# Kernel optimization log

Measured on AMD Instinct MI355X. Metric: run time of the kernel, lower is better.

The kernel has to match this reference:

```python
import jax, jax.numpy as jnp
import numpy as np

C_IN = 256   # in_channels
D = 256      # hidden_dim
RNN_OUT = 2 * D  # bidir concat
K = 80       # num_classes - 1
B, H, W = 16, 64, 64


def setup_inputs() -> dict:
    key = jax.random.key(0)
    ks = jax.random.split(key, 32)
    sD = 1.0 / np.sqrt(D)
    sR = 1.0 / np.sqrt(RNN_OUT)
    f32 = jnp.float32
    inp = {}
    inp["feat"] = jax.random.normal(ks[0], (B, C_IN, H, W), f32)
    # 1x1 conv projection (acts as per-pixel linear)
    inp["proj_w"] = jax.random.normal(ks[1], (D, C_IN), f32) * sD
    inp["proj_b"] = jnp.zeros((D,), f32)
    # FastRNN forward-direction cell
    inp["Wf"] = jax.random.normal(ks[2], (D, D), f32) * sD
    inp["Uf"] = jax.random.normal(ks[3], (D, D), f32) * sD
    inp["bf"] = jnp.zeros((D,), f32)
    inp["alpha_f"] = jnp.asarray(-3.0, f32)  # sigmoid(-3) ~ 0.05 (FastRNN init)
    inp["beta_f"] = jnp.asarray(3.0, f32)    # sigmoid(3)  ~ 0.95
    # FastRNN backward-direction cell
    inp["Wb"] = jax.random.normal(ks[4], (D, D), f32) * sD
    inp["Ub"] = jax.random.normal(ks[5], (D, D), f32) * sD
    inp["bb"] = jnp.zeros((D,), f32)
    inp["alpha_b"] = jnp.asarray(-3.0, f32)
    inp["beta_b"] = jnp.asarray(3.0, f32)
    # cls MLP: Linear(RNN_OUT,RNN_OUT) -> ReLU -> Linear(RNN_OUT,K)
    inp["cls_w1"] = jax.random.normal(ks[6], (RNN_OUT, RNN_OUT), f32) * sR
    inp["cls_b1"] = jnp.zeros((RNN_OUT,), f32)
    inp["cls_w2"] = jax.random.normal(ks[7], (K, RNN_OUT), f32) * sR
    inp["cls_b2"] = jnp.zeros((K,), f32)
    # reg MLP -> 4
    inp["reg_w1"] = jax.random.normal(ks[8], (RNN_OUT, RNN_OUT), f32) * sR
    inp["reg_b1"] = jnp.zeros((RNN_OUT,), f32)
    inp["reg_w2"] = jax.random.normal(ks[9], (4, RNN_OUT), f32) * sR
    inp["reg_b2"] = jnp.zeros((4,), f32)
    # ctr MLP -> 1
    inp["ctr_w1"] = jax.random.normal(ks[10], (RNN_OUT, RNN_OUT), f32) * sR
    inp["ctr_b1"] = jnp.zeros((RNN_OUT,), f32)
    inp["ctr_w2"] = jax.random.normal(ks[11], (1, RNN_OUT), f32) * sR
    inp["ctr_b2"] = jnp.zeros((1,), f32)
    return inp


def _fastrnn_scan(pre, U, alpha, beta):
    # pre: (S, B, D) = W x_t + b precomputed for all steps
    a = jax.nn.sigmoid(alpha)
    b = jax.nn.sigmoid(beta)
    def step(h, p):
        h_new = a * jnp.tanh(p + h @ U.T) + b * h
        return h_new, h_new
    h0 = jnp.zeros(pre.shape[1:], pre.dtype)
    _, hs = jax.lax.scan(step, h0, pre)
    return hs  # (S, B, D)


def _mlp(h, w1, b1, w2, b2):
    return jax.nn.relu(h @ w1.T + b1) @ w2.T + b2


def reference(feat, proj_w, proj_b, Wf, Uf, bf, alpha_f, beta_f,
              Wb, Ub, bb, alpha_b, beta_b,
              cls_w1, cls_b1, cls_w2, cls_b2,
              reg_w1, reg_b1, reg_w2, reg_b2,
              ctr_w1, ctr_b1, ctr_w2, ctr_b2):
    Bn, C, Hn, Wn = feat.shape
    # 1x1 conv proj then flatten spatial tokens: (B, S, D)
    x = jnp.einsum('bchw,dc->bhwd', feat, proj_w) + proj_b
    x = x.reshape(Bn, Hn * Wn, D)
    # forward-direction FastRNN
    pre_f = (x @ Wf.T + bf).transpose(1, 0, 2)           # (S, B, D)
    h_f = _fastrnn_scan(pre_f, Uf, alpha_f, beta_f).transpose(1, 0, 2)
    # backward-direction FastRNN
    pre_b = (x[:, ::-1] @ Wb.T + bb).transpose(1, 0, 2)
    h_b = _fastrnn_scan(pre_b, Ub, alpha_b, beta_b).transpose(1, 0, 2)[:, ::-1]
    h = jnp.concatenate([h_f, h_b], axis=-1)             # (B, S, 2D)
    cls = _mlp(h, cls_w1, cls_b1, cls_w2, cls_b2)
    reg = _mlp(h, reg_w1, reg_b1, reg_w2, reg_b2)
    ctr = _mlp(h, ctr_w1, ctr_b1, ctr_w2, ctr_b2)
    cls = cls.reshape(Bn, Hn, Wn, K).transpose(0, 3, 1, 2)
    reg = jax.nn.relu(reg.reshape(Bn, Hn, Wn, 4).transpose(0, 3, 1, 2))
    ctr = ctr.reshape(Bn, Hn, Wn, 1).transpose(0, 3, 1, 2)
    return (cls, reg, ctr)
```

## Files before the change

kernel.cpp:

```cpp
#include <hip/hip_runtime.h>
#include <hip/hip_bf16.h>

typedef short bf16x8 __attribute__((ext_vector_type(8)));
typedef float f32x4 __attribute__((ext_vector_type(4)));

__device__ __forceinline__ ushort f2b(float x) {
    __hip_bfloat16 h = __float2bfloat16(x);
    return *reinterpret_cast<ushort*>(&h);
}

__device__ __forceinline__ void gload_lds16(const void* g, void* l) {
    __builtin_amdgcn_global_load_lds(
        (const __attribute__((address_space(1))) void*)g,
        (__attribute__((address_space(3))) void*)l, 16, 0, 0);
}

__global__ __launch_bounds__(256) void prep_mcat(
    const float* __restrict__ proj_w, const float* __restrict__ proj_b,
    const float* __restrict__ Wf, const float* __restrict__ bf_,
    const float* __restrict__ Wb, const float* __restrict__ bb_,
    __hip_bfloat16* __restrict__ Mcat, float* __restrict__ cvec)
{
    int n = blockIdx.x;
    int c = threadIdx.x;
    const float* W    = (n < 256) ? (Wf + n * 256) : (Wb + (n - 256) * 256);
    const float* bias = (n < 256) ? bf_ : bb_;
    float acc = 0.f;
    for (int k = 0; k < 256; ++k)
        acc = fmaf(W[k], proj_w[k * 256 + c], acc);
    Mcat[n * 256 + c] = __float2bfloat16(acc);

    __shared__ float red[256];
    red[c] = W[c] * proj_b[c];
    __syncthreads();
    for (int s = 128; s > 0; s >>= 1) {
        if (c < s) red[c] += red[c + s];
        __syncthreads();
    }
    if (c == 0) cvec[n] = red[0] + bias[n & 255];
}

__global__ __launch_bounds__(256) void prep_weights(
    const float* __restrict__ cls_w1, const float* __restrict__ cls_b1,
    const float* __restrict__ cls_w2, const float* __restrict__ cls_b2,
    const float* __restrict__ reg_w1, const float* __restrict__ reg_b1,
    const float* __restrict__ reg_w2, const float* __restrict__ reg_b2,
    const float* __restrict__ ctr_w1, const float* __restrict__ ctr_b1,
    const float* __restrict__ ctr_w2, const float* __restrict__ ctr_b2,
    __hip_bfloat16* __restrict__ W1cat, float* __restrict__ b1cat,
    __hip_bfloat16* __restrict__ w2h, float* __restrict__ b2h)
{
    int idx = blockIdx.x * 256 + threadIdx.x;
    if (idx < 786432) {
        int n = idx >> 9, k = idx & 511;
        const float* src = (n < 512) ? cls_w1 : (n < 1024 ? reg_w1 : ctr_w1);
        int nn = n & 511;
        W1cat[idx] = __float2bfloat16(src[nn * 512 + k]);
    }
    if (idx < 65536) {
        int r = idx >> 9, k = idx & 511;
        float v = 0.f;
        if (r < 80)       v = cls_w2[r * 512 + k];
        else if (r < 84)  v = reg_w2[(r - 80) * 512 + k];
        else if (r == 96) v = ctr_w2[k];
        w2h[idx] = __float2bfloat16(v);
    }
    if (idx < 1536)
        b1cat[idx] = (idx < 512) ? cls_b1[idx] : (idx < 1024 ? reg_b1[idx - 512] : ctr_b1[idx - 1024]);
    if (idx < 112)
        b2h[idx] = (idx < 80) ? cls_b2[idx] : (idx < 84 ? reg_b2[idx - 80] : (idx == 96 ? ctr_b2[0] : 0.f));
}

__global__ __launch_bounds__(256) void transpose_feat(
    const float* __restrict__ feat, __hip_bfloat16* __restrict__ fx)
{
    __shared__ float tile[32][65];
    int st = blockIdx.x * 64, ct = blockIdx.y * 32, b = blockIdx.z;
    int tid = threadIdx.x;
    int sl = tid & 63, cl = tid >> 6;
    const float* fp = feat + ((size_t)b * 256 + ct) * 4096 + st;
#pragma unroll
    for (int i = 0; i < 8; ++i)
        tile[cl + i * 4][sl] = fp[(size_t)(cl + i * 4) * 4096 + sl];
    __syncthreads();
    int cw = tid & 31, sw = tid >> 5;
#pragma unroll
    for (int i = 0; i < 8; ++i) {
        int ss = st + sw + i * 8;
        fx[((size_t)ss * 16 + b) * 256 + ct + cw] = __float2bfloat16(tile[cw][sw + i * 8]);
    }
}

template <int MODE>
__global__ __launch_bounds__(256) void gemm_bf16(
    const __hip_bfloat16* __restrict__ A, const __hip_bfloat16* __restrict__ B,
    void* __restrict__ Cv, const float* __restrict__ bias, int M, int N, int K)
{
    __shared__ __align__(16) ushort As[128][64];
    __shared__ __align__(16) ushort Bs[128][64];
    const int tid = threadIdx.x;
    const int wv = tid >> 6;
    const int lane = tid & 63;
    const int wm = wv >> 1, wn = wv & 1;
    const int l15 = lane & 15, l4 = lane >> 4;
    const int m0 = blockIdx.y * 128;
    const int n0 = blockIdx.x * 128;

    f32x4 acc[4][4];
#pragma unroll
    for (int i = 0; i < 4; ++i)
#pragma unroll
        for (int j = 0; j < 4; ++j) acc[i][j] = (f32x4){0.f, 0.f, 0.f, 0.f};

    const int c0 = wv * 4 * 64 + lane;
    const ushort* Abase = (const ushort*)A;
    const ushort* Bbase = (const ushort*)B;

    for (int k0 = 0; k0 < K; k0 += 64) {
#pragma unroll
        for (int i = 0; i < 4; ++i) {
            int c = c0 + i * 64;
            int row = c >> 3, kc = c & 7;
            int kcs = (kc ^ (row & 7)) * 8;
            gload_lds16(Abase + (size_t)(m0 + row) * K + k0 + kcs,
                        &As[0][0] + (wv * 4 + i) * 512);
            gload_lds16(Bbase + (size_t)(n0 + row) * K + k0 + kcs,
                        &Bs[0][0] + (wv * 4 + i) * 512);
        }
        asm volatile("s_waitcnt vmcnt(0)" ::: "memory");
        __syncthreads();

#pragma unroll
        for (int ks = 0; ks < 2; ++ks) {
            const int swz = ((ks * 4 + l4) ^ (l15 & 7)) * 8;
            bf16x8 af[4], bf[4];
#pragma unroll
            for (int mi = 0; mi < 4; ++mi)
                af[mi] = *(const bf16x8*)(&As[0][0] + (wm * 64 + mi * 16 + l15) * 64 + swz);
#pragma unroll
            for (int ni = 0; ni < 4; ++ni)
                bf[ni] = *(const bf16x8*)(&Bs[0][0] + (wn * 64 + ni * 16 + l15) * 64 + swz);
#pragma unroll
            for (int mi = 0; mi < 4; ++mi)
#pragma unroll
                for (int ni = 0; ni < 4; ++ni)
                    acc[mi][ni] = __builtin_amdgcn_mfma_f32_16x16x32_bf16(af[mi], bf[ni], acc[mi][ni], 0, 0, 0);
        }
        __syncthreads();
    }

#pragma unroll
    for (int mi = 0; mi < 4; ++mi) {
#pragma unroll
        for (int ni = 0; ni < 4; ++ni) {
            int col = n0 + wn * 64 + ni * 16 + l15;
#pragma unroll
            for (int r = 0; r < 4; ++r) {
                int row = m0 + wm * 64 + mi * 16 + l4 * 4 + r;
                float v = acc[mi][ni][r];
                if constexpr (MODE >= 1) v += bias[col];
                if constexpr (MODE == 2) {
                    v = fmaxf(v, 0.f);
                    ((__hip_bfloat16*)Cv)[(size_t)row * N + col] = __float2bfloat16(v);
                } else {
                    ((float*)Cv)[(size_t)row * N + col] = v;
                }
            }
        }
    }
}

__global__ __launch_bounds__(512) void fused_l2(
    const __hip_bfloat16* __restrict__ L1c, const __hip_bfloat16* __restrict__ w2h,
    const float* __restrict__ b2h, float* __restrict__ out, int chunk)
{
    __shared__ __align__(16) char smem[256 * 105 * 4];
    ushort* As = (ushort*)smem;
    ushort* Bs = (ushort*)(smem + 32768);
    float* sacc = (float*)smem;

    const int tid = threadIdx.x;
    const int wv = tid >> 6;
    const int lane = tid & 63;
    const int l15 = lane & 15, l4 = lane >> 4;
    const int tok0 = blockIdx.x * 256;
    const ushort* Ab = (const ushort*)L1c;
    const ushort* Bb = (const ushort*)w2h;

    f32x4 acc[2][7];
#pragma unroll
    for (int i = 0; i < 2; ++i)
#pragma unroll
        for (int j = 0; j < 7; ++j) acc[i][j] = (f32x4){0.f, 0.f, 0.f, 0.f};

#pragma unroll
    for (int p = 0; p < 3; ++p) {
        for (int k0 = 0; k0 < 512; k0 += 64) {
#pragma unroll
            for (int i = 0; i < 4; ++i) {
                int c = (wv * 4 + i) * 64 + lane;
                int row = c >> 3, kc = c & 7;
                int kcs = (kc ^ (row & 7)) * 8;
                gload_lds16(Ab + (size_t)(tok0 + row) * 1536 + p * 512 + k0 + kcs, As + c * 8);
            }
#pragma unroll
            for (int i = 0; i < 2; ++i) {
                int c = (wv * 2 + i) * 64 + lane;
                int row = c >> 3, kc = c & 7;
                int kcs = (kc ^ (row & 7)) * 8;
                gload_lds16(Bb + (size_t)row * 512 + k0 + kcs, Bs + c * 8);
            }
            asm volatile("s_waitcnt vmcnt(0)" ::: "memory");
            __syncthreads();

#pragma unroll
            for (int ks = 0; ks < 2; ++ks) {
                const int swz = ((ks * 4 + l4) ^ (l15 & 7)) * 8;
                bf16x8 af0 = *(const bf16x8*)(As + (wv * 32 + l15) * 64 + swz);
                bf16x8 af1 = *(const bf16x8*)(As + (wv * 32 + 16 + l15) * 64 + swz);
                if (p == 0) {
#pragma unroll
                    for (int ni = 0; ni < 5; ++ni) {
                        bf16x8 bf = *(const bf16x8*)(Bs + (ni * 16 + l15) * 64 + swz);
                        acc[0][ni] = __builtin_amdgcn_mfma_f32_16x16x32_bf16(af0, bf, acc[0][ni], 0, 0, 0);
                        acc[1][ni] = __builtin_amdgcn_mfma_f32_16x16x32_bf16(af1, bf, acc[1][ni], 0, 0, 0);
                    }
                } else {
                    const int ni = (p == 1) ? 5 : 6;
                    bf16x8 bf = *(const bf16x8*)(Bs + (ni * 16 + l15) * 64 + swz);
                    acc[0][ni] = __builtin_amdgcn_mfma_f32_16x16x32_bf16(af0, bf, acc[0][ni], 0, 0, 0);
                    acc[1][ni] = __builtin_amdgcn_mfma_f32_16x16x32_bf16(af1, bf, acc[1][ni], 0, 0, 0);
                }
            }
            __syncthreads();
        }
    }

#pragma unroll
    for (int mi = 0; mi < 2; ++mi) {
#pragma unroll
        for (int ni = 0; ni < 7; ++ni) {
            const int fragcol = ni * 16 + l15;
            const float bias = b2h[fragcol];
#pragma unroll
            for (int r = 0; r < 4; ++r) {
                int row = wv * 32 + mi * 16 + l4 * 4 + r;
                float v = acc[mi][ni][r] + bias;
                if (ni == 5 && l15 < 4) v = fmaxf(v, 0.f);
                if (ni < 6) sacc[row * 105 + fragcol] = v;
                else if (l15 == 0) sacc[row * 105 + 96] = v;
            }
        }
    }
    __syncthreads();

    const int s0 = chunk * 2048 + blockIdx.x * 16;
#pragma unroll
    for (int it = 0; it < 10; ++it) {
        int slot = it * 512 + tid;
        int j = slot >> 6;
        int rem = slot & 63;
        int b = rem >> 2, q = rem & 3;
        float4 v;
#pragma unroll
        for (int e = 0; e < 4; ++e)
            ((float*)&v)[e] = sacc[((q * 4 + e) * 16 + b) * 105 + j];
        *(float4*)(out + (size_t)b * 327680 + (size_t)j * 4096 + s0 + q * 4) = v;
    }
    if (tid < 256) {
        int j = tid >> 6, rem = tid & 63, b = rem >> 2, q = rem & 3;
        float4 v;
#pragma unroll
        for (int e = 0; e < 4; ++e)
            ((float*)&v)[e] = sacc[((q * 4 + e) * 16 + b) * 105 + 80 + j];
        *(float4*)(out + 5242880 + (size_t)b * 16384 + (size_t)j * 4096 + s0 + q * 4) = v;
    }
    if (tid < 64) {
        int b = tid >> 2, q = tid & 3;
        float4 v;
#pragma unroll
        for (int e = 0; e < 4; ++e)
            ((float*)&v)[e] = sacc[((q * 4 + e) * 16 + b) * 105 + 96];
        *(float4*)(out + 5505024 + (size_t)b * 4096 + s0 + q * 4) = v;
    }
}

#define HROW 264
#define CHUNK_S 32
#define WARMUP 192
__global__ __launch_bounds__(512, 2) void scan_chunk(
    const float* __restrict__ pre, const float* __restrict__ Uf, const float* __restrict__ Ub,
    const float* __restrict__ alpha_f, const float* __restrict__ beta_f,
    const float* __restrict__ alpha_b, const float* __restrict__ beta_b,
    __hip_bfloat16* __restrict__ h_out)
{
    const int dir = blockIdx.y;
    const int chk = blockIdx.x;
    const int o0 = chk * CHUNK_S;
    const int o1 = o0 + CHUNK_S;
    int start = o0 - WARMUP; if (start < 0) start = 0;

    const int tid = threadIdx.x;
    const int w = tid >> 6;
    const int lane = tid & 63;
    const int l15 = lane & 15;
    const int l4 = lane >> 4;

    const float* U = dir ? Ub : Uf;
    const float alpha = dir ? alpha_b[0] : alpha_f[0];
    const float beta  = dir ? beta_b[0]  : beta_f[0];
    const float a  = 1.f / (1.f + __expf(-alpha));
    const float bd = 1.f / (1.f + __expf(-beta));

    bf16x8 ufr[2][8];
#pragma unroll
    for (int mt = 0; mt < 2; ++mt) {
        const int row = w * 32 + mt * 16 + l15;
#pragma unroll
        for (int kc = 0; kc < 8; ++kc) {
            const float* up = U + (size_t)row * 256 + kc * 32 + l4 * 8;
            bf16x8 fr;
#pragma unroll
            for (int j = 0; j < 8; ++j) fr[j] = (short)f2b(up[j]);
            ufr[mt][kc] = fr;
        }
    }

    __shared__ __align__(16) ushort hbuf[2][16][HROW];
    for (int i = tid; i < 2 * 16 * HROW; i += 512) ((ushort*)hbuf)[i] = 0;

    float4 hown[2];
    hown[0] = (float4){0.f, 0.f, 0.f, 0.f};
    hown[1] = (float4){0.f, 0.f, 0.f, 0.f};

    const size_t off0 = (size_t)l15 * 512 + dir * 256 + w * 32 + l4 * 4;

    const int wb = tid >> 5;
    const int wp = tid & 31;
    ushort* hob = (ushort*)h_out + dir * 256 + (size_t)wb * 512 + wp * 8;

    const int sA0 = dir ? (4095 - start) : start;
    const int sB0 = dir ? (4095 - (start + 1)) : (start + 1);
    float4 pA0 = *(const float4*)(pre + (size_t)sA0 * 8192 + off0);
    float4 pA1 = *(const float4*)(pre + (size_t)sA0 * 8192 + off0 + 16);
    float4 pB0 = *(const float4*)(pre + (size_t)sB0 * 8192 + off0);
    float4 pB1 = *(const float4*)(pre + (size_t)sB0 * 8192 + off0 + 16);

    __syncthreads();

#define SCAN_STEP(T, CUR, NXT, P0, P1)                                              \
    do {                                                                            \
        const int s_ = dir ? (4095 - (T)) : (T);                                    \
        bf16x8 bfrag[8];                                                            \
        _Pragma("unroll")                                                           \
        for (int kc = 0; kc < 8; ++kc)                                              \
            bfrag[kc] = *(const bf16x8*)&hbuf[CUR][l15][kc * 32 + l4 * 8];          \
        f32x4 acc0 = (f32x4){0.f, 0.f, 0.f, 0.f};                                   \
        f32x4 acc1 = (f32x4){0.f, 0.f, 0.f, 0.f};                                   \
        _Pragma("unroll")                                                           \
        for (int kc = 0; kc < 8; ++kc) {                                            \
            acc0 = __builtin_amdgcn_mfma_f32_16x16x32_bf16(ufr[0][kc], bfrag[kc], acc0, 0, 0, 0); \
            acc1 = __builtin_amdgcn_mfma_f32_16x16x32_bf16(ufr[1][kc], bfrag[kc], acc1, 0, 0, 0); \
        }                                                                           \
        _Pragma("unroll")                                                           \
        for (int mt = 0; mt < 2; ++mt) {                                            \
            f32x4 accv = mt ? acc1 : acc0;                                          \
            const float* pcp = mt ? (const float*)&(P1) : (const float*)&(P0);      \
            const float* hop_ = (const float*)&hown[mt];                            \
            float hn[4];                                                            \
            _Pragma("unroll")                                                       \
            for (int r = 0; r < 4; ++r) {                                           \
                float z = accv[r] + pcp[r];                                         \
                float e = exp2f(z * 2.885390081777927f);                            \
                float th = fmaf(-2.f, __builtin_amdgcn_rcpf(e + 1.f), 1.f);         \
                hn[r] = fmaf(a, th, bd * hop_[r]);                                  \
            }                                                                       \
            hown[mt] = (float4){hn[0], hn[1], hn[2], hn[3]};                        \
            ushort4 pk;                                                             \
            pk.x = f2b(hn[0]); pk.y = f2b(hn[1]); pk.z = f2b(hn[2]); pk.w = f2b(hn[3]); \
            *(ushort4*)&hbuf[NXT][l15][w * 32 + mt * 16 + l4 * 4] = pk;             \
        }                                                                           \
        asm volatile("s_waitcnt lgkmcnt(0)" ::: "memory");                          \
        __builtin_amdgcn_s_barrier();                                               \
        if ((T) >= o0) {                                                            \
            bf16x8 hv = *(const bf16x8*)&hbuf[NXT][wb][wp * 8];                     \
            *(bf16x8*)(hob + (size_t)s_ * 8192) = hv;                               \
        }                                                                           \
    } while (0)

    for (int t = start; t < o1; t += 2) {
        SCAN_STEP(t, 0, 1, pA0, pA1);
        {
            int t2 = (t + 2 < o1) ? (t + 2) : (o1 - 1);
            int s2 = dir ? (4095 - t2) : t2;
            pA0 = *(const float4*)(pre + (size_t)s2 * 8192 + off0);
            pA1 = *(const float4*)(pre + (size_t)s2 * 8192 + off0 + 16);
        }
        SCAN_STEP(t + 1, 1, 0, pB0, pB1);
        {
            int t3 = (t + 3 < o1) ? (t + 3) : (o1 - 1);
            int s3 = dir ? (4095 - t3) : t3;
            pB0 = *(const float4*)(pre + (size_t)s3 * 8192 + off0);
            pB1 = *(const float4*)(pre + (size_t)s3 * 8192 + off0 + 16);
        }
    }
#undef SCAN_STEP
}

extern "C" void kernel_launch(void* const* d_in, const int* in_sizes, int n_in,
                              void* d_out, int out_size, void* d_ws, size_t ws_size,
                              hipStream_t stream) {
    (void)in_sizes; (void)n_in; (void)out_size; (void)ws_size;
    const float* feat    = (const float*)d_in[0];
    const float* proj_w  = (const float*)d_in[1];
    const float* proj_b  = (const float*)d_in[2];
    const float* Wf      = (const float*)d_in[3];
    const float* Uf      = (const float*)d_in[4];
    const float* bf_     = (const float*)d_in[5];
    const float* alpha_f = (const float*)d_in[6];
    const float* beta_f  = (const float*)d_in[7];
    const float* Wb      = (const float*)d_in[8];
    const float* Ub      = (const float*)d_in[9];
    const float* bb_     = (const float*)d_in[10];
    const float* alpha_b = (const float*)d_in[11];
    const float* beta_b  = (const float*)d_in[12];
    const float* cls_w1  = (const float*)d_in[13];
    const float* cls_b1  = (const float*)d_in[14];
    const float* cls_w2  = (const float*)d_in[15];
    const float* cls_b2  = (const float*)d_in[16];
    const float* reg_w1  = (const float*)d_in[17];
    const float* reg_b1  = (const float*)d_in[18];
    const float* reg_w2  = (const float*)d_in[19];
    const float* reg_b2  = (const float*)d_in[20];
    const float* ctr_w1  = (const float*)d_in[21];
    const float* ctr_b1  = (const float*)d_in[22];
    const float* ctr_w2  = (const float*)d_in[23];
    const float* ctr_b2  = (const float*)d_in[24];

    char* ws = (char*)d_ws;
    __hip_bfloat16* h_bf  = (__hip_bfloat16*)(ws);
    float*          pre   = (float*)(ws + 67108864);
    __hip_bfloat16* L1c   = (__hip_bfloat16*)(ws + 67108864);
    char*           regC  = ws + 201326592;
    __hip_bfloat16* fx    = (__hip_bfloat16*)regC;
    char*           wts   = ws + 260046848;
    __hip_bfloat16* Mcat  = (__hip_bfloat16*)(wts);
    float*          cvec  = (float*)(wts + 262144);
    __hip_bfloat16* W1cat = (__hip_bfloat16*)(wts + 264192);
    float*          b1cat = (float*)(wts + 1837056);
    __hip_bfloat16* w2h   = (__hip_bfloat16*)(wts + 1843200);
    float*          b2h   = (float*)(wts + 1974272);

    prep_mcat<<<512, 256, 0, stream>>>(proj_w, proj_b, Wf, bf_, Wb, bb_, Mcat, cvec);
    prep_weights<<<3072, 256, 0, stream>>>(cls_w1, cls_b1, cls_w2, cls_b2,
        reg_w1, reg_b1, reg_w2, reg_b2, ctr_w1, ctr_b1, ctr_w2, ctr_b2,
        W1cat, b1cat, w2h, b2h);
    transpose_feat<<<dim3(64, 8, 16), 256, 0, stream>>>(feat, fx);

    gemm_bf16<1><<<dim3(4, 512), 256, 0, stream>>>(fx, Mcat, pre, cvec, 65536, 512, 256);

    scan_chunk<<<dim3(128, 2), 512, 0, stream>>>(pre, Uf, Ub, alpha_f, beta_f, alpha_b, beta_b, h_bf);

    for (int c = 0; c < 2; ++c) {
        gemm_bf16<2><<<dim3(12, 256), 256, 0, stream>>>(
            h_bf + (size_t)c * 32768 * 512, W1cat, L1c, b1cat, 32768, 1536, 512);
        fused_l2<<<128, 512, 0, stream>>>(L1c, w2h, b2h, (float*)d_out, c);
    }
}
```

Before: 467.1 us.

## Add 256x256-tile pipelined bf16 GEMM with fused ReLU for MLP layer 1

Replaces the generic 128x128-tile GEMM for the first MLP layer with a dedicated 512-thread kernel that uses 256x256 output tiles, XOR-swizzled LDS staging through direct global-to-LDS loads, half-tile double buffering interleaved with MFMA phases, and a workgroup index swizzle for L2 locality. The goal is more data reuse per LDS load and better overlap of global loads with MFMA compute on the dominant GEMM (32768x1536x512, run twice). In exchange it holds many more accumulator registers and relies on hand-placed waitcnt and barrier scheduling, which is fragile.

```diff
diff --git a/kernel.cpp b/kernel.cpp
--- a/kernel.cpp
+++ b/kernel.cpp
@@ -165,6 +165,136 @@
                 } else {
                     ((float*)Cv)[(size_t)row * N + col] = v;
                 }
+            }
+        }
+    }
+}
+
+__global__ __launch_bounds__(512, 2) void gemm256_relu(
+    const __hip_bfloat16* __restrict__ A, const __hip_bfloat16* __restrict__ B,
+    __hip_bfloat16* __restrict__ C, const float* __restrict__ bias, int N, int K)
+{
+    __shared__ __align__(16) ushort Asm[2][2][128][64];
+    __shared__ __align__(16) ushort Bsm[2][2][128][64];
+    const int tid = threadIdx.x;
+    const int wv = tid >> 6;
+    const int lane = tid & 63;
+    const int wqm = wv >> 2, wqn = wv & 3;
+    const int l15 = lane & 15, l4 = lane >> 4;
+    const int nt = K >> 6;
+
+    const int nbx = gridDim.x;
+    int wg = blockIdx.y * nbx + blockIdx.x;
+    int cpx = (nbx * gridDim.y) >> 3;
+    int swz = (wg & 7) * cpx + (wg >> 3);
+    const int m0 = (swz / nbx) * 256;
+    const int n0 = (swz % nbx) * 256;
+
+    f32x4 acc[8][4];
+#pragma unroll
+    for (int i = 0; i < 8; ++i)
+#pragma unroll
+        for (int j = 0; j < 4; ++j) acc[i][j] = (f32x4){0.f, 0.f, 0.f, 0.f};
+
+    const ushort* Ab = (const ushort*)A;
+    const ushort* Bb = (const ushort*)B;
+
+#define STG_HALF(MEM, P, G0, TILE, HALF)                                            \
+    do { if ((TILE) < nt) {                                                         \
+        ushort* db_ = &MEM[(TILE) & 1][HALF][0][0];                                 \
+        _Pragma("unroll")                                                           \
+        for (int i_ = 0; i_ < 2; ++i_) {                                            \
+            int c_ = (wv * 2 + i_) * 64 + lane;                                     \
+            int r_ = c_ >> 3, kc_ = c_ & 7;                                         \
+            int kcs_ = (kc_ ^ (r_ & 7)) * 8;                                        \
+            gload_lds16(P + (size_t)((G0) + (HALF) * 128 + r_) * K + (TILE) * 64 + kcs_, \
+                        db_ + c_ * 8);                                              \
+        } } } while (0)
+
+#define PH(DBUF, MH, NH, ENDW, ...)                                                 \
+    do {                                                                            \
+        bf16x8 afr[2][4], bfr[2][2];                                                \
+        _Pragma("unroll")                                                           \
+        for (int ks_ = 0; ks_ < 2; ++ks_) {                                         \
+            _Pragma("unroll")                                                       \
+            for (int fm_ = 0; fm_ < 4; ++fm_) {                                     \
+                int r_ = wqm * 64 + fm_ * 16 + l15;                                 \
+                afr[ks_][fm_] = *(const bf16x8*)&Asm[DBUF][MH][r_][((ks_ * 4 + l4) ^ (r_ & 7)) * 8]; \
+            }                                                                       \
+            _Pragma("unroll")                                                       \
+            for (int fn_ = 0; fn_ < 2; ++fn_) {                                     \
+                int r_ = wqn * 32 + fn_ * 16 + l15;                                 \
+                bfr[ks_][fn_] = *(const bf16x8*)&Bsm[DBUF][NH][r_][((ks_ * 4 + l4) ^ (r_ & 7)) * 8]; \
+            }                                                                       \
+        }                                                                           \
+        __VA_ARGS__;                                                                \
+        asm volatile("" ::: "memory");                                              \
+        __builtin_amdgcn_s_barrier();                                               \
+        asm volatile("s_waitcnt lgkmcnt(0)" ::: "memory");                          \
+        __builtin_amdgcn_sched_barrier(0);                                          \
+        __builtin_amdgcn_s_setprio(1);                                              \
+        _Pragma("unroll")                                                           \
+        for (int ks_ = 0; ks_ < 2; ++ks_)                                           \
+            _Pragma("unroll")                                                       \
+            for (int fm_ = 0; fm_ < 4; ++fm_)                                       \
+                _Pragma("unroll")                                                   \
+                for (int fn_ = 0; fn_ < 2; ++fn_)                                   \
+                    acc[(MH) * 4 + fm_][(NH) * 2 + fn_] =                           \
+                        __builtin_amdgcn_mfma_f32_16x16x32_bf16(                    \
+                            afr[ks_][fm_], bfr[ks_][fn_],                           \
+                            acc[(MH) * 4 + fm_][(NH) * 2 + fn_], 0, 0, 0);          \
+        __builtin_amdgcn_s_setprio(0);                                              \
+        ENDW;                                                                       \
+        asm volatile("" ::: "memory");                                              \
+        __builtin_amdgcn_s_barrier();                                               \
+        asm volatile("" ::: "memory");                                              \
+    } while (0)
+
+#define VMW_STEADY asm volatile("s_waitcnt vmcnt(4)" ::: "memory")
+#define VMW_TAIL   asm volatile("s_waitcnt vmcnt(0)" ::: "memory")
+
+    STG_HALF(Asm, Ab, m0, 0, 0);
+    STG_HALF(Bsm, Bb, n0, 0, 0);
+    STG_HALF(Asm, Ab, m0, 0, 1);
+    STG_HALF(Bsm, Bb, n0, 0, 1);
+    STG_HALF(Asm, Ab, m0, 1, 0);
+    STG_HALF(Bsm, Bb, n0, 1, 0);
+    asm volatile("s_waitcnt vmcnt(4)" ::: "memory");
+    asm volatile("" ::: "memory");
+    __builtin_amdgcn_s_barrier();
+    asm volatile("" ::: "memory");
+
+    const int niter = nt >> 1;
+    for (int i = 0; i < niter; ++i) {
+        const int U = 2 * i, V = U + 1;
+        const bool tailA = (U + 2 >= nt), tailB = (V + 2 >= nt);
+        PH(0, 0, 0, , STG_HALF(Asm, Ab, m0, V, 1); STG_HALF(Bsm, Bb, n0, V, 1));
+        PH(0, 0, 1, , );
+        PH(0, 1, 0, , STG_HALF(Asm, Ab, m0, U + 2, 0));
+        if (tailA) { PH(0, 1, 1, VMW_TAIL, STG_HALF(Bsm, Bb, n0, U + 2, 0)); }
+        else       { PH(0, 1, 1, VMW_STEADY, STG_HALF(Bsm, Bb, n0, U + 2, 0)); }
+        PH(1, 0, 0, , STG_HALF(Asm, Ab, m0, U + 2, 1); STG_HALF(Bsm, Bb, n0, U + 2, 1));
+        PH(1, 0, 1, , );
+        PH(1, 1, 0, , STG_HALF(Asm, Ab, m0, V + 2, 0));
+        if (tailB) { PH(1, 1, 1, VMW_TAIL, STG_HALF(Bsm, Bb, n0, V + 2, 0)); }
+        else       { PH(1, 1, 1, VMW_STEADY, STG_HALF(Bsm, Bb, n0, V + 2, 0)); }
+    }
+#undef PH
+#undef STG_HALF
+#undef VMW_STEADY
+#undef VMW_TAIL
+
+#pragma unroll
+    for (int am = 0; am < 8; ++am) {
+#pragma unroll
+        for (int an = 0; an < 4; ++an) {
+            int col = n0 + (an >> 1) * 128 + wqn * 32 + (an & 1) * 16 + l15;
+            int row0 = m0 + (am >> 2) * 128 + wqm * 64 + (am & 3) * 16 + l4 * 4;
+            float bv = bias[col];
+#pragma unroll
+            for (int r = 0; r < 4; ++r) {
+                float v = fmaxf(acc[am][an][r] + bv, 0.f);
+                C[(size_t)(row0 + r) * N + col] = __float2bfloat16(v);
             }
         }
     }
@@ -462,8 +592,8 @@
     scan_chunk<<<dim3(128, 2), 512, 0, stream>>>(pre, Uf, Ub, alpha_f, beta_f, alpha_b, beta_b, h_bf);
 
     for (int c = 0; c < 2; ++c) {
-        gemm_bf16<2><<<dim3(12, 256), 256, 0, stream>>>(
-            h_bf + (size_t)c * 32768 * 512, W1cat, L1c, b1cat, 32768, 1536, 512);
+        gemm256_relu<<<dim3(6, 128), 512, 0, stream>>>(
+            h_bf + (size_t)c * 32768 * 512, W1cat, L1c, b1cat, 1536, 512);
         fused_l2<<<128, 512, 0, stream>>>(L1c, w2h, b2h, (float*)d_out, c);
     }
 }
```

Result: no change. 468.7 us (+0.3%).
